# Kernel optimization log

Hardware: AMD Instinct MI355X
Metric: run time of the kernel (lower is better)

Reference implementation:

```python
import jax, jax.numpy as jnp
import numpy as np

B, S, OBS, H, A = 256, 128, 256, 1024, 18


def setup_inputs() -> dict:
    key = jax.random.key(0)
    ks = jax.random.split(key, 12)
    sc = lambda fan_in: 1.0 / np.sqrt(fan_in)
    u = lambda k, shape, s: jax.random.uniform(k, shape, jnp.float32, -s, s)
    return {
        "obs": jax.random.normal(ks[0], (B, S, OBS), jnp.float32),
        "hx": jnp.zeros((B, H), jnp.float32),
        "cx": jnp.zeros((B, H), jnp.float32),
        "behaviour_acts": jax.random.randint(ks[1], (B, S, 1), 0, A, jnp.int32),
        "W_body": u(ks[2], (H, OBS), sc(OBS)),
        "b_body": u(ks[3], (H,), sc(OBS)),
        "W_ih": u(ks[4], (4 * H, H), sc(H)),
        "b_ih": u(ks[5], (4 * H,), sc(H)),
        "W_hh": u(ks[6], (4 * H, H), sc(H)),
        "b_hh": u(ks[7], (4 * H,), sc(H)),
        "W_v": u(ks[8], (1, H), sc(H)),
        "b_v": u(ks[9], (1,), sc(H)),
        "W_l": u(ks[10], (A, H), sc(H)),
        "b_l": u(ks[11], (A,), sc(H)),
    }


def reference(obs, hx, cx, behaviour_acts, W_body, b_body, W_ih, b_ih,
              W_hh, b_hh, W_v, b_v, W_l, b_l):
    acts = behaviour_acts.astype(jnp.int32).squeeze(-1)  # [B,S]
    # body MLP: Linear + ReLU
    x = jax.nn.relu(jnp.einsum("bso,ho->bsh", obs, W_body) + b_body)  # [B,S,H]
    # precompute input-to-gate contributions for all timesteps (batched GEMM)
    xg = jnp.einsum("bsh,gh->bsg", x, W_ih) + b_ih  # [B,S,4H]
    xg_t = jnp.swapaxes(xg, 0, 1)  # [S,B,4H]

    def step(carry, g_in):
        h, c = carry
        g = g_in + h @ W_hh.T + b_hh  # [B,4H]
        i, f, gg, o = jnp.split(g, 4, axis=-1)  # torch LSTMCell gate order i,f,g,o
        i = jax.nn.sigmoid(i)
        f = jax.nn.sigmoid(f)
        gg = jnp.tanh(gg)
        o = jax.nn.sigmoid(o)
        c = f * c + i * gg
        h = o * jnp.tanh(c)
        return (h, c), h

    _, hs = jax.lax.scan(step, (hx, cx), xg_t)  # hs: [S,B,H]
    hs = jnp.swapaxes(hs, 0, 1)  # [B,S,H]

    value = jnp.einsum("bsh,vh->bsv", hs, W_v) + b_v  # [B,S,1]
    logits = jnp.einsum("bsh,ah->bsa", hs, W_l) + b_l  # [B,S,A]
    # Categorical(probs=softmax(logits)): dist.logits == log_softmax(logits)
    logp = jax.nn.log_softmax(logits, axis=-1)  # [B,S,A]
    log_prob = jnp.take_along_axis(logp, acts[..., None], axis=-1)  # [B,S,1]
    entropy = -jnp.sum(jnp.exp(logp) * logp, axis=-1, keepdims=True)  # [B,S,1]
    return logp, log_prob, entropy, value
```

## Files before the change

### kernel.cpp

```cpp
#include <hip/hip_runtime.h>

#define AS1 __attribute__((address_space(1)))
#define AS3 __attribute__((address_space(3)))

typedef __attribute__((ext_vector_type(4))) float f32x4;
typedef __attribute__((ext_vector_type(8))) short s16x8;
typedef __attribute__((ext_vector_type(4))) short s16x4;

static constexpr int BB = 256, SS = 128, OBSN = 256, HH = 1024, AN = 18;
static constexpr int MM = BB * SS;
static constexpr int G4 = 4 * HH;

static constexpr int LP_OFF  = MM * AN;
static constexpr int ENT_OFF = LP_OFF + MM;
static constexpr int VAL_OFF = ENT_OFF + MM;

__device__ __forceinline__ short f2bf(float f) {
  unsigned u = __builtin_bit_cast(unsigned, f);
  u += 0x7FFFu + ((u >> 16) & 1u);
  return (short)(u >> 16);
}
__device__ __forceinline__ float bf2f(short s) {
  unsigned u = ((unsigned)(unsigned short)s) << 16;
  return __builtin_bit_cast(float, u);
}
__device__ __forceinline__ void gl_lds16(const void* g, void* l) {
  __builtin_amdgcn_global_load_lds((const AS1 void*)g, (AS3 void*)l, 16, 0, 0);
}
__device__ __forceinline__ float sigf(float x) {
  x = fminf(fmaxf(x, -30.f), 30.f);
  return 1.f / (1.f + __expf(-x));
}
__device__ __forceinline__ float tanhfast(float x) {
  x = fminf(fmaxf(x, -15.f), 15.f);
  float e = __expf(2.f * x);
  return (e - 1.f) / (e + 1.f);
}
__device__ __forceinline__ void cast4(const float* __restrict__ s,
                                      short* __restrict__ d, int i) {
  f32x4 v = ((const f32x4*)s)[i];
  s16x4 o;
  o[0] = f2bf(v[0]); o[1] = f2bf(v[1]); o[2] = f2bf(v[2]); o[3] = f2bf(v[3]);
  ((s16x4*)d)[i] = o;
}

__global__ __launch_bounds__(256) void prep(
    const float* __restrict__ obs, const float* __restrict__ Wb,
    const float* __restrict__ Wih, const float* __restrict__ Whh,
    const float* __restrict__ Wl, const float* __restrict__ Wv,
    const float* __restrict__ bih, const float* __restrict__ bhh,
    const float* __restrict__ hx, const float* __restrict__ cx,
    short* __restrict__ obsb, short* __restrict__ wbo, short* __restrict__ wiho,
    short* __restrict__ whho, short* __restrict__ wlo, short* __restrict__ wvo,
    float* __restrict__ bsum, short* __restrict__ h0o, float* __restrict__ co) {
  int i = blockIdx.x * 256 + threadIdx.x;
  if (i < 2097152) { cast4(obs, obsb, i); return; }
  i -= 2097152;
  if (i < 65536) { cast4(Wb, wbo, i); return; }
  i -= 65536;
  if (i < 1048576) { cast4(Wih, wiho, i); return; }
  i -= 1048576;
  if (i < 1048576) { cast4(Whh, whho, i); return; }
  i -= 1048576;
  if (i < 4608) { cast4(Wl, wlo, i); return; }
  i -= 4608;
  if (i < 256) { cast4(Wv, wvo, i); return; }
  i -= 256;
  if (i < 1024) {
    f32x4 a = ((const f32x4*)bih)[i];
    f32x4 b = ((const f32x4*)bhh)[i];
    ((f32x4*)bsum)[i] = a + b;
    return;
  }
  i -= 1024;
  cast4(hx, h0o, i);
  ((f32x4*)co)[i] = ((const f32x4*)cx)[i];
}

template <int N, int K, bool RELU, int REMAP>
__global__ __launch_bounds__(256, 2) void gemm_bt(
    const short* __restrict__ A, const short* __restrict__ Bw,
    const float* __restrict__ bias, short* __restrict__ C, int t0) {
  __shared__ short lA[128 * 32];
  __shared__ short lB[128 * 32];
  const int tid = threadIdx.x;
  const int lane = tid & 63, wave = tid >> 6;
  const int nTN = N / 128;
  const int tm = blockIdx.x / nTN, tn = blockIdx.x % nTN;

  const int r0 = tid >> 2;
  const int kc = (tid & 3) * 8;

  const int m0 = tm * 128 + r0;
  const int m1 = m0 + 64;
  size_t pr0, pr1;
  if constexpr (REMAP == 1) {
    pr0 = (size_t)((m0 & (BB - 1)) * SS + t0 + (m0 >> 8));
    pr1 = (size_t)((m1 & (BB - 1)) * SS + t0 + (m1 >> 8));
  } else {
    pr0 = (size_t)m0; pr1 = (size_t)m1;
  }
  const short* a0 = A + pr0 * K + kc;
  const short* a1 = A + pr1 * K + kc;
  const short* b0 = Bw + (size_t)(tn * 128 + r0) * K + kc;
  const short* b1 = Bw + (size_t)(tn * 128 + r0 + 64) * K + kc;

  f32x4 acc[4][4];
#pragma unroll
  for (int i = 0; i < 4; ++i)
#pragma unroll
    for (int j = 0; j < 4; ++j) acc[i][j] = {0.f, 0.f, 0.f, 0.f};

  const int wr = (wave >> 1) * 64;
  const int wc = (wave & 1) * 64;
  const int fr = lane & 15;
  const int fk = (lane >> 4) * 8;

  for (int k0 = 0; k0 < K; k0 += 32) {
    __syncthreads();
    gl_lds16(a0 + k0, &lA[tid * 8]);
    gl_lds16(a1 + k0, &lA[2048 + tid * 8]);
    gl_lds16(b0 + k0, &lB[tid * 8]);
    gl_lds16(b1 + k0, &lB[2048 + tid * 8]);
    __syncthreads();
    s16x8 af[4], bfr[4];
#pragma unroll
    for (int i = 0; i < 4; ++i)
      af[i] = *(const s16x8*)&lA[(wr + i * 16 + fr) * 32 + fk];
#pragma unroll
    for (int j = 0; j < 4; ++j)
      bfr[j] = *(const s16x8*)&lB[(wc + j * 16 + fr) * 32 + fk];
#pragma unroll
    for (int i = 0; i < 4; ++i)
#pragma unroll
      for (int j = 0; j < 4; ++j)
        acc[i][j] = __builtin_amdgcn_mfma_f32_16x16x32_bf16(af[i], bfr[j], acc[i][j], 0, 0, 0);
  }

  const int orow = (lane >> 4) * 4;
#pragma unroll
  for (int i = 0; i < 4; ++i) {
#pragma unroll
    for (int j = 0; j < 4; ++j) {
      const int colg = tn * 128 + wc + j * 16 + fr;
      const float bv = bias[colg];
#pragma unroll
      for (int r = 0; r < 4; ++r) {
        const int rowg = tm * 128 + wr + i * 16 + orow + r;
        float v = acc[i][j][r] + bv;
        if (RELU) v = v > 0.f ? v : 0.f;
        C[(size_t)rowg * N + colg] = f2bf(v);
      }
    }
  }
}

__global__ __launch_bounds__(256, 2) void lstm_step(
    const short* __restrict__ h_in, short* __restrict__ h_out,
    float* __restrict__ cst, const short* __restrict__ Whh,
    const short* __restrict__ xg_s,
    short* __restrict__ hs_s) {
  __shared__ char smem[40960];
  float* lG = (float*)smem;
  short* smS = (short*)smem;

  const int tid = threadIdx.x, lane = tid & 63, wave = tid >> 6;
  const int bt = blockIdx.x >> 5, ht = blockIdx.x & 31;
  const int b0 = bt * 32, h0 = ht * 32;

  const int lq = lane >> 4;
  const int lc = lane & 15;

  const short* wsrc[8];
  {
    const size_t rowbase = (size_t)(wave * HH + h0 + lq) * HH;
#pragma unroll
    for (int q = 0; q < 8; ++q)
      wsrc[q] = Whh + rowbase + (size_t)q * 4 * HH +
                (size_t)((lc ^ (((q & 1) << 2) | lq)) * 8);
  }
  const short* hsrc[4];
  {
    const size_t rowbase = (size_t)(b0 + (wave & 1) * 16 + lq) * HH;
#pragma unroll
    for (int q = 0; q < 4; ++q)
      hsrc[q] = h_in + rowbase + (size_t)q * 4 * HH +
                (size_t)((lc ^ (((q & 1) << 2) | lq)) * 8);
  }

  const int fr = lane & 15;
  f32x4 acc[2][2];
#pragma unroll
  for (int i = 0; i < 2; ++i)
#pragma unroll
    for (int j = 0; j < 2; ++j) acc[i][j] = {0.f, 0.f, 0.f, 0.f};

  for (int it = 0; it < 8; ++it) {
    const int k0 = it * 128;
    __syncthreads();
#pragma unroll
    for (int q = 0; q < 8; ++q)
      gl_lds16(wsrc[q] + k0, &smS[4096 + wave * 4096 + q * 512 + lane * 8]);
    if (wave < 2) {
#pragma unroll
      for (int q = 0; q < 4; ++q)
        gl_lds16(hsrc[q] + k0, &smS[wave * 2048 + q * 512 + lane * 8]);
    }
    __syncthreads();
#pragma unroll
    for (int kk = 0; kk < 4; ++kk) {
      const int sw = ((kk * 4 + lq) ^ (fr & 7)) * 8;
      s16x8 ha[2], wb[2];
#pragma unroll
      for (int i = 0; i < 2; ++i)
        ha[i] = *(const s16x8*)&smS[(i * 16 + fr) * 128 + sw];
#pragma unroll
      for (int j = 0; j < 2; ++j)
        wb[j] = *(const s16x8*)&smS[4096 + wave * 4096 + (j * 16 + fr) * 128 + sw];
#pragma unroll
      for (int i = 0; i < 2; ++i)
#pragma unroll
        for (int j = 0; j < 2; ++j)
          acc[i][j] = __builtin_amdgcn_mfma_f32_16x16x32_bf16(ha[i], wb[j], acc[i][j], 0, 0, 0);
    }
  }
  __syncthreads();
#pragma unroll
  for (int i = 0; i < 2; ++i)
#pragma unroll
    for (int j = 0; j < 2; ++j)
#pragma unroll
      for (int r = 0; r < 4; ++r) {
        const int row = i * 16 + lq * 4 + r;
        const int col = j * 16 + fr;
        lG[wave * 1024 + row * 32 + col] = acc[i][j][r];
      }
  __syncthreads();

  const int er = tid >> 3, cb = (tid & 7) * 4;
  const int b = b0 + er;
  const size_t xgb = (size_t)b * G4 + h0 + cb;
  const s16x4 xi = *(const s16x4*)&xg_s[xgb];
  const s16x4 xf = *(const s16x4*)&xg_s[xgb + HH];
  const s16x4 xc = *(const s16x4*)&xg_s[xgb + 2 * HH];
  const s16x4 xo = *(const s16x4*)&xg_s[xgb + 3 * HH];
  const size_t cib = (size_t)b * HH + h0 + cb;
  f32x4 cv = *(const f32x4*)&cst[cib];
  s16x4 hb;
#pragma unroll
  for (int q = 0; q < 4; ++q) {
    const int col = cb + q;
    const float gi = lG[0 * 1024 + er * 32 + col] + bf2f(xi[q]);
    const float gf = lG[1 * 1024 + er * 32 + col] + bf2f(xf[q]);
    const float gc = lG[2 * 1024 + er * 32 + col] + bf2f(xc[q]);
    const float go = lG[3 * 1024 + er * 32 + col] + bf2f(xo[q]);
    const float iv = sigf(gi), fv = sigf(gf), gv = tanhfast(gc), ov = sigf(go);
    const float cn = fv * cv[q] + iv * gv;
    cv[q] = cn;
    hb[q] = f2bf(ov * tanhfast(cn));
  }
  *(f32x4*)&cst[cib] = cv;
  *(s16x4*)&h_out[cib] = hb;
  *(s16x4*)&hs_s[cib] = hb;
}

__global__ __launch_bounds__(256) void heads_k(
    const short* __restrict__ hs, const short* __restrict__ Wl,
    const float* __restrict__ bl, const short* __restrict__ Wv,
    const float* __restrict__ bv, const int* __restrict__ acts,
    float* __restrict__ out, int t0) {
  const int tid = threadIdx.x, lane = tid & 63, wave = tid >> 6;
  const int r = blockIdx.x * 4 + wave;
  const int sl = r >> 8, b = r & 255;
  const int mg = b * SS + t0 + sl;
  const short* hrow = hs + (size_t)r * HH + lane * 16;
  const s16x8 hv0 = *(const s16x8*)hrow;
  const s16x8 hv1 = *(const s16x8*)(hrow + 8);
  float xv[16];
#pragma unroll
  for (int e = 0; e < 8; ++e) { xv[e] = bf2f(hv0[e]); xv[8 + e] = bf2f(hv1[e]); }

  float lg[19];
#pragma unroll
  for (int j = 0; j < 19; ++j) {
    const short* wp = (j < 18 ? Wl + (size_t)j * HH : Wv) + lane * 16;
    const s16x8 w0 = *(const s16x8*)wp;
    const s16x8 w1 = *(const s16x8*)(wp + 8);
    float s = 0.f;
#pragma unroll
    for (int e = 0; e < 8; ++e) s += xv[e] * bf2f(w0[e]) + xv[8 + e] * bf2f(w1[e]);
#pragma unroll
    for (int d = 32; d >= 1; d >>= 1) s += __shfl_xor(s, d, 64);
    lg[j] = s + (j < 18 ? bl[j] : bv[0]);
  }
  float mx = lg[0];
#pragma unroll
  for (int j = 1; j < 18; ++j) mx = fmaxf(mx, lg[j]);
  float se = 0.f;
#pragma unroll
  for (int j = 0; j < 18; ++j) se += __expf(lg[j] - mx);
  const float lse = __logf(se);
  if (lane == 0) {
    const int act = acts[mg];
    float ent = 0.f, sel = 0.f;
#pragma unroll
    for (int j = 0; j < 18; ++j) {
      const float lp = lg[j] - mx - lse;
      out[(size_t)mg * 18 + j] = lp;
      ent -= __expf(lp) * lp;
      if (j == act) sel = lp;
    }
    out[LP_OFF + mg] = sel;
    out[ENT_OFF + mg] = ent;
    out[VAL_OFF + mg] = lg[18];
  }
}

extern "C" void kernel_launch(void* const* d_in, const int* in_sizes, int n_in,
                              void* d_out, int out_size, void* d_ws, size_t ws_size,
                              hipStream_t stream) {
  const float* obs    = (const float*)d_in[0];
  const float* hx     = (const float*)d_in[1];
  const float* cx     = (const float*)d_in[2];
  const int*   acts   = (const int*)d_in[3];
  const float* W_body = (const float*)d_in[4];
  const float* b_body = (const float*)d_in[5];
  const float* W_ih   = (const float*)d_in[6];
  const float* b_ih   = (const float*)d_in[7];
  const float* W_hh   = (const float*)d_in[8];
  const float* b_hh   = (const float*)d_in[9];
  const float* W_v    = (const float*)d_in[10];
  const float* b_v    = (const float*)d_in[11];
  const float* W_l    = (const float*)d_in[12];
  const float* b_l    = (const float*)d_in[13];
  float* out = (float*)d_out;
  (void)in_sizes; (void)n_in; (void)out_size;

  const size_t FIXED = 36231168ull;
  const size_t PER_C = 3145728ull;
  int chunk = 16;
  while (chunk > 1 && FIXED + (size_t)chunk * PER_C > ws_size) chunk >>= 1;

  char* ws = (char*)d_ws;
  size_t off = 0;
  auto give = [&](size_t bytes) -> char* {
    char* p = ws + off;
    off += (bytes + 255) & ~(size_t)255;
    return p;
  };
  short* wb   = (short*)give((size_t)HH * OBSN * 2);
  short* wih  = (short*)give((size_t)G4 * HH * 2);
  short* whh  = (short*)give((size_t)G4 * HH * 2);
  short* wl   = (short*)give((size_t)AN * HH * 2);
  short* wv   = (short*)give((size_t)HH * 2);
  float* bsum = (float*)give((size_t)G4 * 4);
  short* obsb = (short*)give((size_t)MM * OBSN * 2);
  short* h0b  = (short*)give((size_t)BB * HH * 2);
  short* h1b  = (short*)give((size_t)BB * HH * 2);
  float* cbuf = (float*)give((size_t)BB * HH * 4);
  short* xc   = (short*)give((size_t)chunk * BB * HH * 2);
  short* xgc  = (short*)give((size_t)chunk * BB * G4 * 2);
  short* hsc  = (short*)give((size_t)chunk * BB * HH * 2);

  prep<<<16919, 256, 0, stream>>>(obs, W_body, W_ih, W_hh, W_l, W_v, b_ih, b_hh,
                                  hx, cx, obsb, wb, wih, whh, wl, wv, bsum, h0b, cbuf);

  short* ha = h0b;
  short* hb = h1b;
  const int Mc = chunk * BB;
  for (int t0 = 0; t0 < SS; t0 += chunk) {
    gemm_bt<HH, OBSN, true, 1>
        <<<(Mc / 128) * (HH / 128), 256, 0, stream>>>(obsb, wb, b_body, xc, t0);
    gemm_bt<G4, HH, false, 0>
        <<<(Mc / 128) * (G4 / 128), 256, 0, stream>>>(xc, wih, bsum, xgc, 0);
    for (int sl = 0; sl < chunk; ++sl) {
      lstm_step<<<256, 256, 0, stream>>>(ha, hb, cbuf, whh,
                                         xgc + (size_t)sl * BB * G4,
                                         hsc + (size_t)sl * BB * HH);
      short* t = ha; ha = hb; hb = t;
    }
    heads_k<<<Mc / 4, 256, 0, stream>>>(hsc, wl, b_l, wv, b_v, acts, out, t0);
  }
}
```

Baseline: 1.822 ms.

## Replace per-step LSTM launches with persistent scan kernel using grid barrier

Per-timestep lstm_step launches are replaced by a persistent lstm_scan kernel that runs a whole chunk of timesteps. Each block keeps its slice of W_hh (128 KB) resident in LDS. Blocks of the same batch tile synchronize through an atomic counter barrier in global memory, and h is double-buffered through LDS. This removes per-step launch overhead and repeated W_hh reloads, but relies on all 256 blocks being co-resident and spin-waiting. There is a possible hazard: hprev for a later chunk points into hsc, which the scan overwrites while other blocks may still be reading it.

Result: slower. 2.476 ms (+35.9%).

```diff
diff --git a/kernel.cpp b/kernel.cpp
--- a/kernel.cpp
+++ b/kernel.cpp
@@ -155,113 +155,102 @@
   }
 }
 
-__global__ __launch_bounds__(256, 2) void lstm_step(
-    const short* __restrict__ h_in, short* __restrict__ h_out,
-    float* __restrict__ cst, const short* __restrict__ Whh,
-    const short* __restrict__ xg_s,
-    short* __restrict__ hs_s) {
-  __shared__ char smem[40960];
-  float* lG = (float*)smem;
-  short* smS = (short*)smem;
-
-  const int tid = threadIdx.x, lane = tid & 63, wave = tid >> 6;
-  const int bt = blockIdx.x >> 5, ht = blockIdx.x & 31;
-  const int b0 = bt * 32, h0 = ht * 32;
-
-  const int lq = lane >> 4;
-  const int lc = lane & 15;
-
-  const short* wsrc[8];
-  {
-    const size_t rowbase = (size_t)(wave * HH + h0 + lq) * HH;
-#pragma unroll
-    for (int q = 0; q < 8; ++q)
-      wsrc[q] = Whh + rowbase + (size_t)q * 4 * HH +
-                (size_t)((lc ^ (((q & 1) << 2) | lq)) * 8);
-  }
-  const short* hsrc[4];
-  {
-    const size_t rowbase = (size_t)(b0 + (wave & 1) * 16 + lq) * HH;
-#pragma unroll
-    for (int q = 0; q < 4; ++q)
-      hsrc[q] = h_in + rowbase + (size_t)q * 4 * HH +
-                (size_t)((lc ^ (((q & 1) << 2) | lq)) * 8);
-  }
-
-  const int fr = lane & 15;
-  f32x4 acc[2][2];
-#pragma unroll
-  for (int i = 0; i < 2; ++i)
-#pragma unroll
-    for (int j = 0; j < 2; ++j) acc[i][j] = {0.f, 0.f, 0.f, 0.f};
-
-  for (int it = 0; it < 8; ++it) {
-    const int k0 = it * 128;
+static __device__ __forceinline__ void stage_h(const short* hsrc, int b0, int kc,
+                                               char* dst, int tid) {
+#pragma unroll
+  for (int rd = 0; rd < 2; ++rd) {
+    const int cid = rd * 256 + tid;
+    const int r = cid >> 3, cp = cid & 7;
+    gl_lds16(hsrc + (size_t)(b0 + r) * HH + kc * 64 + ((cp ^ (r & 7)) << 3),
+             dst + cid * 16);
+  }
+}
+
+__global__ __launch_bounds__(256, 1) void lstm_scan(
+    const short* __restrict__ Whh, const short* __restrict__ xg,
+    short* __restrict__ hs, const short* __restrict__ h0,
+    float* __restrict__ cst, int* __restrict__ bar, int nsteps, int bar_base) {
+  extern __shared__ char smem[];
+  short* lW = (short*)smem;
+  char* lHa = smem + 131072;
+  char* lHb = smem + 131072 + 8192;
+
+  const int tid = threadIdx.x, lane = tid & 63, w = tid >> 6;
+  const int bt = blockIdx.x >> 6, ht = blockIdx.x & 63;
+  const int b0 = bt * 64, hc0 = ht * 16;
+  const int fr = lane & 15, fh = lane >> 4;
+
+#pragma unroll 4
+  for (int j = 0; j < 32; ++j) {
+    const int cid = j * 256 + tid;
+    const int r = cid >> 7, cp = cid & 127;
+    const int wrow = (r >> 4) * HH + hc0 + (r & 15);
+    gl_lds16(Whh + (size_t)wrow * HH + ((cp ^ (r & 7)) << 3), smem + cid * 16);
+  }
+  const int brow = b0 + w * 16 + fh * 4;
+  const int hcol = hc0 + fr;
+  float cv[4];
+#pragma unroll
+  for (int r = 0; r < 4; ++r) cv[r] = cst[(size_t)(brow + r) * HH + hcol];
+
+  int* cnt = bar + bt * 64;
+
+  for (int sl = 0; sl < nsteps; ++sl) {
+    const short* hsrc = (sl == 0) ? h0 : hs + (size_t)(sl - 1) * (BB * HH);
+    float xgv[4][4];
+    {
+      const short* xgb = xg + (size_t)sl * BB * G4;
+#pragma unroll
+      for (int j = 0; j < 4; ++j)
+#pragma unroll
+        for (int r = 0; r < 4; ++r)
+          xgv[j][r] = bf2f(xgb[(size_t)(brow + r) * G4 + j * HH + hcol]);
+    }
+    f32x4 acc[4];
+#pragma unroll
+    for (int j = 0; j < 4; ++j) acc[j] = {0.f, 0.f, 0.f, 0.f};
+
+    stage_h(hsrc, b0, 0, lHa, tid);
+    for (int kc = 0; kc < 16; ++kc) {
+      __syncthreads();
+      if (kc < 15) stage_h(hsrc, b0, kc + 1, (kc & 1) ? lHa : lHb, tid);
+      const char* cur = (kc & 1) ? lHb : lHa;
+#pragma unroll
+      for (int kk = 0; kk < 2; ++kk) {
+        const int c = kk * 4 + fh;
+        const int arow = w * 16 + fr;
+        const s16x8 af = *(const s16x8*)(cur + arow * 128 + ((c ^ (arow & 7)) << 4));
+#pragma unroll
+        for (int j = 0; j < 4; ++j) {
+          const int wr2 = j * 16 + fr;
+          const s16x8 bfr = *(const s16x8*)((const char*)lW + wr2 * 2048 +
+                                            (((kc * 8 + c) ^ (wr2 & 7)) << 4));
+          acc[j] = __builtin_amdgcn_mfma_f32_16x16x32_bf16(af, bfr, acc[j], 0, 0, 0);
+        }
+      }
+    }
+    short* hdst = hs + (size_t)sl * (BB * HH);
+#pragma unroll
+    for (int r = 0; r < 4; ++r) {
+      const float gi = acc[0][r] + xgv[0][r];
+      const float gf = acc[1][r] + xgv[1][r];
+      const float gc = acc[2][r] + xgv[2][r];
+      const float go = acc[3][r] + xgv[3][r];
+      const float cn = sigf(gf) * cv[r] + sigf(gi) * tanhfast(gc);
+      cv[r] = cn;
+      hdst[(size_t)(brow + r) * HH + hcol] = f2bf(sigf(go) * tanhfast(cn));
+    }
     __syncthreads();
-#pragma unroll
-    for (int q = 0; q < 8; ++q)
-      gl_lds16(wsrc[q] + k0, &smS[4096 + wave * 4096 + q * 512 + lane * 8]);
-    if (wave < 2) {
-#pragma unroll
-      for (int q = 0; q < 4; ++q)
-        gl_lds16(hsrc[q] + k0, &smS[wave * 2048 + q * 512 + lane * 8]);
+    if (tid == 0) {
+      __hip_atomic_fetch_add(cnt, 1, __ATOMIC_RELEASE, __HIP_MEMORY_SCOPE_AGENT);
+      const int target = bar_base + (sl + 1) * 64;
+      while (__hip_atomic_load(cnt, __ATOMIC_ACQUIRE, __HIP_MEMORY_SCOPE_AGENT) < target)
+        __builtin_amdgcn_s_sleep(2);
     }
     __syncthreads();
-#pragma unroll
-    for (int kk = 0; kk < 4; ++kk) {
-      const int sw = ((kk * 4 + lq) ^ (fr & 7)) * 8;
-      s16x8 ha[2], wb[2];
-#pragma unroll
-      for (int i = 0; i < 2; ++i)
-        ha[i] = *(const s16x8*)&smS[(i * 16 + fr) * 128 + sw];
-#pragma unroll
-      for (int j = 0; j < 2; ++j)
-        wb[j] = *(const s16x8*)&smS[4096 + wave * 4096 + (j * 16 + fr) * 128 + sw];
-#pragma unroll
-      for (int i = 0; i < 2; ++i)
-#pragma unroll
-        for (int j = 0; j < 2; ++j)
-          acc[i][j] = __builtin_amdgcn_mfma_f32_16x16x32_bf16(ha[i], wb[j], acc[i][j], 0, 0, 0);
-    }
-  }
-  __syncthreads();
-#pragma unroll
-  for (int i = 0; i < 2; ++i)
-#pragma unroll
-    for (int j = 0; j < 2; ++j)
-#pragma unroll
-      for (int r = 0; r < 4; ++r) {
-        const int row = i * 16 + lq * 4 + r;
-        const int col = j * 16 + fr;
-        lG[wave * 1024 + row * 32 + col] = acc[i][j][r];
-      }
-  __syncthreads();
-
-  const int er = tid >> 3, cb = (tid & 7) * 4;
-  const int b = b0 + er;
-  const size_t xgb = (size_t)b * G4 + h0 + cb;
-  const s16x4 xi = *(const s16x4*)&xg_s[xgb];
-  const s16x4 xf = *(const s16x4*)&xg_s[xgb + HH];
-  const s16x4 xc = *(const s16x4*)&xg_s[xgb + 2 * HH];
-  const s16x4 xo = *(const s16x4*)&xg_s[xgb + 3 * HH];
-  const size_t cib = (size_t)b * HH + h0 + cb;
-  f32x4 cv = *(const f32x4*)&cst[cib];
-  s16x4 hb;
-#pragma unroll
-  for (int q = 0; q < 4; ++q) {
-    const int col = cb + q;
-    const float gi = lG[0 * 1024 + er * 32 + col] + bf2f(xi[q]);
-    const float gf = lG[1 * 1024 + er * 32 + col] + bf2f(xf[q]);
-    const float gc = lG[2 * 1024 + er * 32 + col] + bf2f(xc[q]);
-    const float go = lG[3 * 1024 + er * 32 + col] + bf2f(xo[q]);
-    const float iv = sigf(gi), fv = sigf(gf), gv = tanhfast(gc), ov = sigf(go);
-    const float cn = fv * cv[q] + iv * gv;
-    cv[q] = cn;
-    hb[q] = f2bf(ov * tanhfast(cn));
-  }
-  *(f32x4*)&cst[cib] = cv;
-  *(s16x4*)&h_out[cib] = hb;
-  *(s16x4*)&hs_s[cib] = hb;
+  }
+#pragma unroll
+  for (int r = 0; r < 4; ++r) cst[(size_t)(brow + r) * HH + hcol] = cv[r];
 }
 
 __global__ __launch_bounds__(256) void heads_k(
@@ -336,7 +325,10 @@
   float* out = (float*)d_out;
   (void)in_sizes; (void)n_in; (void)out_size;
 
-  const size_t FIXED = 36231168ull;
+  (void)hipFuncSetAttribute((const void*)lstm_scan,
+                            hipFuncAttributeMaxDynamicSharedMemorySize, 147456);
+
+  const size_t FIXED = 36235264ull;
   const size_t PER_C = 3145728ull;
   int chunk = 16;
   while (chunk > 1 && FIXED + (size_t)chunk * PER_C > ws_size) chunk >>= 1;
@@ -358,27 +350,27 @@
   short* h0b  = (short*)give((size_t)BB * HH * 2);
   short* h1b  = (short*)give((size_t)BB * HH * 2);
   float* cbuf = (float*)give((size_t)BB * HH * 4);
+  int*   barb = (int*)give(1024);
   short* xc   = (short*)give((size_t)chunk * BB * HH * 2);
   short* xgc  = (short*)give((size_t)chunk * BB * G4 * 2);
   short* hsc  = (short*)give((size_t)chunk * BB * HH * 2);
+  (void)h1b;
+
+  hipMemsetAsync(barb, 0, 1024, stream);
 
   prep<<<16919, 256, 0, stream>>>(obs, W_body, W_ih, W_hh, W_l, W_v, b_ih, b_hh,
                                   hx, cx, obsb, wb, wih, whh, wl, wv, bsum, h0b, cbuf);
 
-  short* ha = h0b;
-  short* hb = h1b;
   const int Mc = chunk * BB;
-  for (int t0 = 0; t0 < SS; t0 += chunk) {
+  int launchIdx = 0;
+  for (int t0 = 0; t0 < SS; t0 += chunk, ++launchIdx) {
     gemm_bt<HH, OBSN, true, 1>
         <<<(Mc / 128) * (HH / 128), 256, 0, stream>>>(obsb, wb, b_body, xc, t0);
     gemm_bt<G4, HH, false, 0>
         <<<(Mc / 128) * (G4 / 128), 256, 0, stream>>>(xc, wih, bsum, xgc, 0);
-    for (int sl = 0; sl < chunk; ++sl) {
-      lstm_step<<<256, 256, 0, stream>>>(ha, hb, cbuf, whh,
-                                         xgc + (size_t)sl * BB * G4,
-                                         hsc + (size_t)sl * BB * HH);
-      short* t = ha; ha = hb; hb = t;
-    }
+    const short* hprev = (t0 == 0) ? h0b : hsc + (size_t)(chunk - 1) * BB * HH;
+    lstm_scan<<<256, 256, 147456, stream>>>(whh, xgc, hsc, hprev, cbuf, barb,
+                                            chunk, launchIdx * chunk * 64);
     heads_k<<<Mc / 4, 256, 0, stream>>>(hsc, wl, b_l, wv, b_v, acts, out, t0);
   }
 }
```
